# Kernel optimization log

Hardware: AMD Instinct MI355X
Metric: run time of the kernel (lower is better)

Reference implementation:

```python
import jax, jax.numpy as jnp
import numpy as np

RESO = 192
BASIS_DIM = 8
DATA_DIM = BASIS_DIM * 3 + 4  # 28
N_PTS = 2_000_000


def setup_inputs() -> dict:
    key = jax.random.key(0)
    k1, k2 = jax.random.split(key)
    # world-space points within the grid radius [-1, 1]^3
    points = jax.random.uniform(k1, (N_PTS, 3), jnp.float32, -1.0, 1.0)
    data = jax.random.normal(k2, (RESO ** 3, DATA_DIM), jnp.float32) * 0.1
    links = jnp.arange(RESO ** 3, dtype=jnp.int32).reshape(RESO, RESO, RESO)
    # _offset = 0.5*(1 - center/radius) = 0.5 ; _scaling = 0.5/radius = 0.5
    offset = jnp.full((3,), 0.5, jnp.float32)
    scaling = jnp.full((3,), 0.5, jnp.float32)
    return {"points": points, "data": data, "links": links,
            "offset": offset, "scaling": scaling}


def _fetch(data, links, ix, iy, iz):
    # sparse indirection: link < 0 means empty voxel -> all-zero channels
    lk = links[ix, iy, iz]                       # (N,) int32
    vals = data[jnp.clip(lk, 0)]                 # (N, C)
    return jnp.where((lk >= 0)[:, None], vals, 0.0)


def reference(points, data, links, offset, scaling):
    gsz_f = jnp.asarray(links.shape, jnp.float32)   # (3,)
    gsz_i = jnp.asarray(links.shape, jnp.int32)
    # world2grid then clamp to [0, size-1] (border padding, align_corners=False)
    pts = points * (scaling * gsz_f) + (offset * gsz_f - 0.5)
    pts = jnp.clip(pts, 0.0, gsz_f - 1.0)
    l = jnp.clip(pts.astype(jnp.int32), 0, gsz_i - 2)  # lower corner, (N,3)
    wb = pts - l.astype(jnp.float32)                   # frac weights
    wa = 1.0 - wb
    lx, ly, lz = l[:, 0], l[:, 1], l[:, 2]

    c000 = _fetch(data, links, lx, ly, lz)
    c001 = _fetch(data, links, lx, ly, lz + 1)
    c010 = _fetch(data, links, lx, ly + 1, lz)
    c011 = _fetch(data, links, lx, ly + 1, lz + 1)
    c100 = _fetch(data, links, lx + 1, ly, lz)
    c101 = _fetch(data, links, lx + 1, ly, lz + 1)
    c110 = _fetch(data, links, lx + 1, ly + 1, lz)
    c111 = _fetch(data, links, lx + 1, ly + 1, lz + 1)

    wz_a, wz_b = wa[:, 2:3], wb[:, 2:3]
    c00 = c000 * wz_a + c001 * wz_b
    c01 = c010 * wz_a + c011 * wz_b
    c10 = c100 * wz_a + c101 * wz_b
    c11 = c110 * wz_a + c111 * wz_b
    c0 = c00 * wa[:, 1:2] + c01 * wb[:, 1:2]
    c1 = c10 * wa[:, 1:2] + c11 * wb[:, 1:2]
    samples = c0 * wa[:, 0:1] + c1 * wb[:, 0:1]        # (N, 28)
    return samples
```

## Files before the change

### kernel.cpp

```cpp
#include <hip/hip_runtime.h>
#include <stdint.h>

#define RESO 192
#define NVOX (RESO * RESO * RESO)
#define DATA_DIM 28
#define CHUNKS 7
#define TPA 12
#define NT 1728
#define NXCD 8
#define TPX 216
#define BLOCKS_P 256

#define AS1 __attribute__((address_space(1)))
#define AS3 __attribute__((address_space(3)))


__device__ __forceinline__ float4 f4_lerp(float4 a, float4 b, float wa, float wb) {
    float4 r;
    r.x = fmaf(a.x, wa, b.x * wb);
    r.y = fmaf(a.y, wa, b.y * wb);
    r.z = fmaf(a.z, wa, b.z * wb);
    r.w = fmaf(a.w, wa, b.w * wb);
    return r;
}

__device__ __forceinline__ int point_coords(
    const float* __restrict__ points,
    const float* __restrict__ offset,
    const float* __restrict__ scaling,
    int p, int* l, float* wb)
{
    int t = 0;
#pragma unroll
    for (int i = 0; i < 3; ++i) {
        float v = fmaf(points[(size_t)p * 3 + i], scaling[i] * (float)RESO,
                       offset[i] * (float)RESO - 0.5f);
        v = fminf(fmaxf(v, 0.0f), (float)RESO - 1.0f);
        int li = (int)v;
        if (li > RESO - 2) li = RESO - 2;
        l[i] = li;
        wb[i] = v - (float)li;
        t = t * TPA + (li >> 4);
    }
    return t;
}

__device__ __forceinline__ float4 trilerp8(const float4* cv, float4 pw) {
    const float waz = 1.0f - pw.z, wbz = pw.z;
    const float way = 1.0f - pw.y, wby = pw.y;
    const float wax = 1.0f - pw.x, wbx = pw.x;
    float4 c00 = f4_lerp(cv[0], cv[1], waz, wbz);
    float4 c01 = f4_lerp(cv[2], cv[3], waz, wbz);
    float4 c10 = f4_lerp(cv[4], cv[5], waz, wbz);
    float4 c11 = f4_lerp(cv[6], cv[7], waz, wbz);
    float4 c0 = f4_lerp(c00, c01, way, wby);
    float4 c1 = f4_lerp(c10, c11, way, wby);
    return f4_lerp(c0, c1, wax, wbx);
}


__global__ void k_init_flag(int* __restrict__ flag) {
    if (threadIdx.x == 0) flag[0] = 1;
}

__global__ __launch_bounds__(256) void k_check_links(
    const int* __restrict__ links, int* __restrict__ flag)
{
    bool ok = true;
    for (int i = blockIdx.x * 256 + threadIdx.x; i < NVOX; i += gridDim.x * 256)
        ok &= (links[i] == i);
    if (!ok) atomicAnd(flag, 0);
}


__global__ __launch_bounds__(256) void k_hist(
    const float* __restrict__ points,
    const float* __restrict__ offset,
    const float* __restrict__ scaling,
    int* __restrict__ ghist,
    int n, int ppb)
{
    __shared__ int lh[NT];
    for (int i = threadIdx.x; i < NT; i += 256) lh[i] = 0;
    __syncthreads();
    const int b = blockIdx.x;
    const int lo = b * ppb;
    const int hi = min(lo + ppb, n);
    for (int p = lo + threadIdx.x; p < hi; p += 256) {
        int l[3]; float wb[3];
        const int t = point_coords(points, offset, scaling, p, l, wb);
        atomicAdd(&lh[t], 1);
    }
    __syncthreads();
    for (int i = threadIdx.x; i < NT; i += 256)
        ghist[(size_t)i * BLOCKS_P + b] = lh[i];
}

__global__ __launch_bounds__(256) void k_rowsum(
    const int* __restrict__ ghist, int* __restrict__ binsum)
{
    const int wave = (blockIdx.x * 256 + threadIdx.x) >> 6;
    const int lane = threadIdx.x & 63;
    if (wave >= NT) return;
    const int* row = ghist + (size_t)wave * BLOCKS_P;
    int s = 0;
#pragma unroll
    for (int i = 0; i < BLOCKS_P / 64; ++i) s += row[lane + i * 64];
#pragma unroll
    for (int d = 32; d > 0; d >>= 1) s += __shfl_xor(s, d, 64);
    if (lane == 0) binsum[wave] = s;
}

__global__ __launch_bounds__(1024) void k_scan_bins(
    const int* __restrict__ binsum, int* __restrict__ csum)
{
    __shared__ int buf[2][2048];
    for (int t = threadIdx.x; t < 2048; t += 1024)
        buf[0][t] = (t < NT) ? binsum[t] : 0;
    __syncthreads();
    int src = 0;
    for (int d = 1; d < 2048; d <<= 1) {
        for (int t = threadIdx.x; t < 2048; t += 1024)
            buf[src ^ 1][t] = buf[src][t] + (t >= d ? buf[src][t - d] : 0);
        __syncthreads();
        src ^= 1;
    }
    for (int t = threadIdx.x; t < NT; t += 1024)
        csum[t] = t ? buf[src][t - 1] : 0;
    if (threadIdx.x == 0) csum[NT] = buf[src][NT - 1];
}

__global__ __launch_bounds__(256) void k_scan_blocks(
    const int* __restrict__ ghist,
    const int* __restrict__ csum,
    int* __restrict__ goff)
{
    const int wave = (blockIdx.x * 256 + threadIdx.x) >> 6;
    const int lane = threadIdx.x & 63;
    if (wave >= NT) return;
    const int* row  = ghist + (size_t)wave * BLOCKS_P;
    int*       orow = goff  + (size_t)wave * BLOCKS_P;
    const int C = BLOCKS_P / 64;
    int v[C], pre[C];
    int lsum = 0;
#pragma unroll
    for (int i = 0; i < C; ++i) {
        v[i] = row[lane * C + i];
        pre[i] = lsum;
        lsum += v[i];
    }
    int incl = lsum;
#pragma unroll
    for (int d = 1; d < 64; d <<= 1) {
        int t = __shfl_up(incl, d, 64);
        if (lane >= d) incl += t;
    }
    const int excl = incl - lsum + csum[wave];
#pragma unroll
    for (int i = 0; i < C; ++i)
        orow[lane * C + i] = excl + pre[i];
}

__global__ __launch_bounds__(256) void k_scatter(
    const float* __restrict__ points,
    const float* __restrict__ offset,
    const float* __restrict__ scaling,
    const int* __restrict__ goff,
    int* __restrict__ perm,
    float4* __restrict__ pre4,
    int n, int ppb)
{
    __shared__ int cur[NT];
    const int b = blockIdx.x;
    for (int i = threadIdx.x; i < NT; i += 256)
        cur[i] = goff[(size_t)i * BLOCKS_P + b];
    __syncthreads();
    const int lo = b * ppb;
    const int hi = min(lo + ppb, n);
    for (int p = lo + threadIdx.x; p < hi; p += 256) {
        int l[3]; float wb[3];
        const int t = point_coords(points, offset, scaling, p, l, wb);
        const int slot = atomicAdd(&cur[t], 1);
        const int gbase = (l[0] * RESO + l[1]) * RESO + l[2];
        perm[slot] = p;
        pre4[slot] = make_float4(wb[0], wb[1], wb[2], __int_as_float(gbase));
    }
}


__global__ __launch_bounds__(256) void k_sample_sorted(
    const int*    __restrict__ perm,
    const float4* __restrict__ pre4,
    const int*    __restrict__ csum,
    const float*  __restrict__ data,
    const int*    __restrict__ links,
    const int*    __restrict__ flag,
    float*        __restrict__ out,
    int bpx)
{
    __shared__ __align__(16) char stage[4 * 8 * 64 * 16];
    char* wbase = stage + (threadIdx.x >> 6) * 8192;
    const int lane = threadIdx.x & 63;

    const int k = blockIdx.x & (NXCD - 1);
    const int j = blockIdx.x >> 3;
    const int lo = csum[k * TPX];
    const int hi = csum[(k + 1) * TPX];
    const int nwork = (hi - lo) * CHUNKS;
    const int stride = bpx * 256;
    const bool fast = (flag[0] != 0);
    const int dz = 1, dy = RESO, dx = RESO * RESO;
    const int offs[8] = {0, dz, dy, dy + dz, dx, dx + dz, dx + dy, dx + dy + dz};

    for (int item = j * 256 + (int)threadIdx.x; item < nwork; item += stride) {
        const int slot = lo + item / CHUNKS;
        const int c    = item % CHUNKS;
        const int p    = perm[slot];
        const float4 pw = pre4[slot];
        const int gbase = __float_as_int(pw.w);

        float4 cv[8];

        if (fast) {
            const float* bA = data + (size_t)c * 4;
#pragma unroll
            for (int q = 0; q < 8; ++q) {
                const float* g = bA + (size_t)(gbase + offs[q]) * DATA_DIM;
                __builtin_amdgcn_global_load_lds(
                    (const AS1 void*)g, (AS3 void*)(wbase + q * 1024), 16, 0, 0);
            }
            asm volatile("s_waitcnt vmcnt(0)" ::: "memory");
#pragma unroll
            for (int q = 0; q < 8; ++q)
                cv[q] = *reinterpret_cast<const float4*>(wbase + q * 1024 + lane * 16);
        } else {
            int lk[8];
#pragma unroll
            for (int q = 0; q < 8; ++q) lk[q] = links[gbase + offs[q]];
#pragma unroll
            for (int q = 0; q < 8; ++q)
                cv[q] = *reinterpret_cast<const float4*>(
                    data + (size_t)(lk[q] < 0 ? 0 : lk[q]) * DATA_DIM + (size_t)c * 4);
#pragma unroll
            for (int q = 0; q < 8; ++q)
                if (lk[q] < 0) cv[q] = make_float4(0.f, 0.f, 0.f, 0.f);
        }

        const float4 s = trilerp8(cv, pw);
        *reinterpret_cast<float4*>(out + (size_t)p * DATA_DIM + (size_t)c * 4) = s;
    }
}


__global__ __launch_bounds__(256) void k_sample_direct(
    const float* __restrict__ points,
    const float* __restrict__ data,
    const int*   __restrict__ links,
    const float* __restrict__ offset,
    const float* __restrict__ scaling,
    float*       __restrict__ out,
    int n_pts)
{
    const int tid = blockIdx.x * blockDim.x + threadIdx.x;
    const int total = n_pts * CHUNKS;
    if (tid >= total) return;
    const int p = tid / CHUNKS;
    const int c = tid - p * CHUNKS;

    int l[3]; float wb[3];
    (void)point_coords(points, offset, scaling, p, l, wb);
    const int gbase = (l[0] * RESO + l[1]) * RESO + l[2];

    const int dz = 1, dy = RESO, dx = RESO * RESO;
    int lk[8];
    lk[0] = links[gbase];
    lk[1] = links[gbase + dz];
    lk[2] = links[gbase + dy];
    lk[3] = links[gbase + dy + dz];
    lk[4] = links[gbase + dx];
    lk[5] = links[gbase + dx + dz];
    lk[6] = links[gbase + dx + dy];
    lk[7] = links[gbase + dx + dy + dz];

    float4 cv[8];
#pragma unroll
    for (int q = 0; q < 8; ++q) {
        const int idx = lk[q] < 0 ? 0 : lk[q];
        cv[q] = *reinterpret_cast<const float4*>(
            data + (size_t)idx * DATA_DIM + (size_t)c * 4);
    }
#pragma unroll
    for (int q = 0; q < 8; ++q)
        if (lk[q] < 0) cv[q] = make_float4(0.f, 0.f, 0.f, 0.f);

    float4 pw = make_float4(wb[0], wb[1], wb[2], 0.f);
    const float4 s = trilerp8(cv, pw);
    *reinterpret_cast<float4*>(out + (size_t)tid * 4) = s;
}


extern "C" void kernel_launch(void* const* d_in, const int* in_sizes, int n_in,
                              void* d_out, int out_size, void* d_ws, size_t ws_size,
                              hipStream_t stream)
{
    const float* points  = (const float*)d_in[0];
    const float* data    = (const float*)d_in[1];
    const int*   links   = (const int*)d_in[2];
    const float* offset  = (const float*)d_in[3];
    const float* scaling = (const float*)d_in[4];
    float*       out     = (float*)d_out;

    const int n_pts = in_sizes[0] / 3;

    size_t off = 0;
    auto alloc = [&](size_t bytes) {
        size_t a = off;
        off = (off + bytes + 255) & ~(size_t)255;
        return a;
    };
    const size_t o_flag   = alloc(4);
    const size_t o_ghist  = alloc((size_t)NT * BLOCKS_P * 4);
    const size_t o_goff   = alloc((size_t)NT * BLOCKS_P * 4);
    const size_t o_binsum = alloc((size_t)NT * 4);
    const size_t o_csum   = alloc((size_t)(NT + 1) * 4);
    const size_t o_perm   = alloc((size_t)n_pts * 4);
    const size_t o_pre4   = alloc((size_t)n_pts * 16);
    const size_t need = off;

    if (ws_size >= need) {
        int*    flag   = (int*)((char*)d_ws + o_flag);
        int*    ghist  = (int*)((char*)d_ws + o_ghist);
        int*    goff   = (int*)((char*)d_ws + o_goff);
        int*    binsum = (int*)((char*)d_ws + o_binsum);
        int*    csum   = (int*)((char*)d_ws + o_csum);
        int*    perm   = (int*)((char*)d_ws + o_perm);
        float4* pre4   = (float4*)((char*)d_ws + o_pre4);

        const int ppb = (n_pts + BLOCKS_P - 1) / BLOCKS_P;

        k_init_flag<<<1, 64, 0, stream>>>(flag);
        k_check_links<<<2048, 256, 0, stream>>>(links, flag);
        k_hist<<<BLOCKS_P, 256, 0, stream>>>(points, offset, scaling, ghist, n_pts, ppb);
        k_rowsum<<<(NT * 64 + 255) / 256, 256, 0, stream>>>(ghist, binsum);
        k_scan_bins<<<1, 1024, 0, stream>>>(binsum, csum);
        k_scan_blocks<<<(NT * 64 + 255) / 256, 256, 0, stream>>>(ghist, csum, goff);
        k_scatter<<<BLOCKS_P, 256, 0, stream>>>(points, offset, scaling, goff,
                                                perm, pre4, n_pts, ppb);

        const long long items_per_xcd =
            ((long long)n_pts * CHUNKS + NXCD - 1) / NXCD;
        const int bpx = (int)((items_per_xcd + 255) / 256);
        k_sample_sorted<<<bpx * NXCD, 256, 0, stream>>>(
            perm, pre4, csum, data, links, flag, out, bpx);
    } else {
        const int total = n_pts * CHUNKS;
        k_sample_direct<<<(total + 255) / 256, 256, 0, stream>>>(
            points, data, links, offset, scaling, out, n_pts);
    }
}
```

Before: 453.6 us.

## Stage 9x9x9 voxel tiles in LDS per fine bin for trilinear sampling

Points are binned into finer 8^3-voxel tiles (13824 bins), and the histogram and offset tables are transposed to a block-major layout. The per-bin scans become one thread per bin. The sampling kernel now runs one block per tile. It loads the tile's 9x9x9 voxel neighbourhood of data into LDS with coalesced float4 loads, then serves all eight corner reads from LDS instead of doing per-point global gathers. The cost is about 81KB of dynamic LDS per block, which limits occupancy, plus redundant halo loads, and the staging is not overlapped with compute.

```diff
diff --git a/kernel.cpp b/kernel.cpp
--- a/kernel.cpp
+++ b/kernel.cpp
@@ -5,14 +5,14 @@
 #define NVOX (RESO * RESO * RESO)
 #define DATA_DIM 28
 #define CHUNKS 7
-#define TPA 12
-#define NT 1728
+#define TPA 24
+#define NBIN 13824
 #define NXCD 8
-#define TPX 216
+#define BPX 1728
 #define BLOCKS_P 256
-
-#define AS1 __attribute__((address_space(1)))
-#define AS3 __attribute__((address_space(3)))
+#define ROWF 252
+#define STAGE_F (81 * ROWF)
+#define STAGE_LD (81 * (ROWF / 4))
 
 
 __device__ __forceinline__ float4 f4_lerp(float4 a, float4 b, float wa, float wb) {
@@ -40,7 +40,7 @@
         if (li > RESO - 2) li = RESO - 2;
         l[i] = li;
         wb[i] = v - (float)li;
-        t = t * TPA + (li >> 4);
+        t = t * TPA + (li >> 3);
     }
     return t;
 }
@@ -80,8 +80,8 @@
     int* __restrict__ ghist,
     int n, int ppb)
 {
-    __shared__ int lh[NT];
-    for (int i = threadIdx.x; i < NT; i += 256) lh[i] = 0;
+    __shared__ int lh[NBIN];
+    for (int i = threadIdx.x; i < NBIN; i += 256) lh[i] = 0;
     __syncthreads();
     const int b = blockIdx.x;
     const int lo = b * ppb;
@@ -92,42 +92,41 @@
         atomicAdd(&lh[t], 1);
     }
     __syncthreads();
-    for (int i = threadIdx.x; i < NT; i += 256)
-        ghist[(size_t)i * BLOCKS_P + b] = lh[i];
+    int* orow = ghist + (size_t)b * NBIN;
+    for (int i = threadIdx.x; i < NBIN; i += 256) orow[i] = lh[i];
 }
 
 __global__ __launch_bounds__(256) void k_rowsum(
     const int* __restrict__ ghist, int* __restrict__ binsum)
 {
-    const int wave = (blockIdx.x * 256 + threadIdx.x) >> 6;
-    const int lane = threadIdx.x & 63;
-    if (wave >= NT) return;
-    const int* row = ghist + (size_t)wave * BLOCKS_P;
+    const int bin = blockIdx.x * 256 + threadIdx.x;
+    if (bin >= NBIN) return;
     int s = 0;
-#pragma unroll
-    for (int i = 0; i < BLOCKS_P / 64; ++i) s += row[lane + i * 64];
-#pragma unroll
-    for (int d = 32; d > 0; d >>= 1) s += __shfl_xor(s, d, 64);
-    if (lane == 0) binsum[wave] = s;
-}
-
-__global__ __launch_bounds__(1024) void k_scan_bins(
+    for (int b = 0; b < BLOCKS_P; ++b) s += ghist[(size_t)b * NBIN + bin];
+    binsum[bin] = s;
+}
+
+__global__ __launch_bounds__(512) void k_scan_bins(
     const int* __restrict__ binsum, int* __restrict__ csum)
 {
-    __shared__ int buf[2][2048];
-    for (int t = threadIdx.x; t < 2048; t += 1024)
-        buf[0][t] = (t < NT) ? binsum[t] : 0;
-    __syncthreads();
-    int src = 0;
-    for (int d = 1; d < 2048; d <<= 1) {
-        for (int t = threadIdx.x; t < 2048; t += 1024)
-            buf[src ^ 1][t] = buf[src][t] + (t >= d ? buf[src][t - d] : 0);
+    __shared__ int vals[NBIN];
+    __shared__ int part[512];
+    const int t = threadIdx.x;
+    const int PER = NBIN / 512;
+    int s = 0;
+    for (int i = 0; i < PER; ++i) { int v = binsum[t * PER + i]; vals[t * PER + i] = v; s += v; }
+    part[t] = s;
+    __syncthreads();
+    for (int d = 1; d < 512; d <<= 1) {
+        int v = part[t];
+        int add = (t >= d) ? part[t - d] : 0;
         __syncthreads();
-        src ^= 1;
-    }
-    for (int t = threadIdx.x; t < NT; t += 1024)
-        csum[t] = t ? buf[src][t - 1] : 0;
-    if (threadIdx.x == 0) csum[NT] = buf[src][NT - 1];
+        part[t] = v + add;
+        __syncthreads();
+    }
+    int run = (t == 0) ? 0 : part[t - 1];
+    for (int i = 0; i < PER; ++i) { int v = vals[t * PER + i]; csum[t * PER + i] = run; run += v; }
+    if (t == 511) csum[NBIN] = run;
 }
 
 __global__ __launch_bounds__(256) void k_scan_blocks(
@@ -135,30 +134,13 @@
     const int* __restrict__ csum,
     int* __restrict__ goff)
 {
-    const int wave = (blockIdx.x * 256 + threadIdx.x) >> 6;
-    const int lane = threadIdx.x & 63;
-    if (wave >= NT) return;
-    const int* row  = ghist + (size_t)wave * BLOCKS_P;
-    int*       orow = goff  + (size_t)wave * BLOCKS_P;
-    const int C = BLOCKS_P / 64;
-    int v[C], pre[C];
-    int lsum = 0;
-#pragma unroll
-    for (int i = 0; i < C; ++i) {
-        v[i] = row[lane * C + i];
-        pre[i] = lsum;
-        lsum += v[i];
-    }
-    int incl = lsum;
-#pragma unroll
-    for (int d = 1; d < 64; d <<= 1) {
-        int t = __shfl_up(incl, d, 64);
-        if (lane >= d) incl += t;
-    }
-    const int excl = incl - lsum + csum[wave];
-#pragma unroll
-    for (int i = 0; i < C; ++i)
-        orow[lane * C + i] = excl + pre[i];
+    const int bin = blockIdx.x * 256 + threadIdx.x;
+    if (bin >= NBIN) return;
+    int run = csum[bin];
+    for (int b = 0; b < BLOCKS_P; ++b) {
+        goff[(size_t)b * NBIN + bin] = run;
+        run += ghist[(size_t)b * NBIN + bin];
+    }
 }
 
 __global__ __launch_bounds__(256) void k_scatter(
@@ -170,10 +152,10 @@
     float4* __restrict__ pre4,
     int n, int ppb)
 {
-    __shared__ int cur[NT];
+    __shared__ int cur[NBIN];
     const int b = blockIdx.x;
-    for (int i = threadIdx.x; i < NT; i += 256)
-        cur[i] = goff[(size_t)i * BLOCKS_P + b];
+    const int* grow = goff + (size_t)b * NBIN;
+    for (int i = threadIdx.x; i < NBIN; i += 256) cur[i] = grow[i];
     __syncthreads();
     const int lo = b * ppb;
     const int hi = min(lo + ppb, n);
@@ -181,59 +163,78 @@
         int l[3]; float wb[3];
         const int t = point_coords(points, offset, scaling, p, l, wb);
         const int slot = atomicAdd(&cur[t], 1);
-        const int gbase = (l[0] * RESO + l[1]) * RESO + l[2];
+        const unsigned lpack = ((unsigned)l[0] << 16) | ((unsigned)l[1] << 8) | (unsigned)l[2];
         perm[slot] = p;
-        pre4[slot] = make_float4(wb[0], wb[1], wb[2], __int_as_float(gbase));
-    }
-}
-
-
-__global__ __launch_bounds__(256) void k_sample_sorted(
+        pre4[slot] = make_float4(wb[0], wb[1], wb[2], __uint_as_float(lpack));
+    }
+}
+
+
+__global__ __launch_bounds__(256) void k_sample_tiled(
     const int*    __restrict__ perm,
     const float4* __restrict__ pre4,
     const int*    __restrict__ csum,
     const float*  __restrict__ data,
     const int*    __restrict__ links,
     const int*    __restrict__ flag,
-    float*        __restrict__ out,
-    int bpx)
-{
-    __shared__ __align__(16) char stage[4 * 8 * 64 * 16];
-    char* wbase = stage + (threadIdx.x >> 6) * 8192;
-    const int lane = threadIdx.x & 63;
-
-    const int k = blockIdx.x & (NXCD - 1);
-    const int j = blockIdx.x >> 3;
-    const int lo = csum[k * TPX];
-    const int hi = csum[(k + 1) * TPX];
-    const int nwork = (hi - lo) * CHUNKS;
-    const int stride = bpx * 256;
+    float*        __restrict__ out)
+{
+    extern __shared__ float lds[];
+
+    const int k   = blockIdx.x & (NXCD - 1);
+    const int j   = blockIdx.x >> 3;
+    const int bin = k * BPX + j;
+    const int bx = bin / (TPA * TPA);
+    const int by = (bin / TPA) % TPA;
+    const int bz = bin % TPA;
+    const int b0x = min(bx * 8, RESO - 9);
+    const int b0y = min(by * 8, RESO - 9);
+    const int b0z = min(bz * 8, RESO - 9);
+
     const bool fast = (flag[0] != 0);
+    const int lo = csum[bin], hi = csum[bin + 1];
+    const int items = (hi - lo) * CHUNKS;
+
+    if (fast) {
+        for (int i = threadIdx.x; i < STAGE_LD; i += 256) {
+            const int pair = i / 63;
+            const int f4   = i - pair * 63;
+            const int gx = b0x + pair / 9;
+            const int gy = b0y + (pair - (pair / 9) * 9);
+            const float* src = data + ((size_t)(gx * RESO + gy) * RESO + b0z) * DATA_DIM
+                             + (size_t)f4 * 4;
+            *reinterpret_cast<float4*>(lds + pair * ROWF + f4 * 4) =
+                *reinterpret_cast<const float4*>(src);
+        }
+    }
+    __syncthreads();
+
+    const int dzf = 28, dyf = ROWF, dxf = 9 * ROWF;
     const int dz = 1, dy = RESO, dx = RESO * RESO;
-    const int offs[8] = {0, dz, dy, dy + dz, dx, dx + dz, dx + dy, dx + dy + dz};
-
-    for (int item = j * 256 + (int)threadIdx.x; item < nwork; item += stride) {
-        const int slot = lo + item / CHUNKS;
-        const int c    = item % CHUNKS;
+
+    for (int i = threadIdx.x; i < items; i += 256) {
+        const int slot = lo + i / CHUNKS;
+        const int c    = i - (i / CHUNKS) * CHUNKS;
         const int p    = perm[slot];
         const float4 pw = pre4[slot];
-        const int gbase = __float_as_int(pw.w);
+        const unsigned lp = __float_as_uint(pw.w);
+        const int lx = lp >> 16, ly = (lp >> 8) & 255, lz = lp & 255;
 
         float4 cv[8];
-
         if (fast) {
-            const float* bA = data + (size_t)c * 4;
-#pragma unroll
-            for (int q = 0; q < 8; ++q) {
-                const float* g = bA + (size_t)(gbase + offs[q]) * DATA_DIM;
-                __builtin_amdgcn_global_load_lds(
-                    (const AS1 void*)g, (AS3 void*)(wbase + q * 1024), 16, 0, 0);
-            }
-            asm volatile("s_waitcnt vmcnt(0)" ::: "memory");
-#pragma unroll
-            for (int q = 0; q < 8; ++q)
-                cv[q] = *reinterpret_cast<const float4*>(wbase + q * 1024 + lane * 16);
+            const float* fb = lds + ((lx - b0x) * 9 + (ly - b0y)) * ROWF
+                            + (lz - b0z) * 28 + c * 4;
+            cv[0] = *reinterpret_cast<const float4*>(fb);
+            cv[1] = *reinterpret_cast<const float4*>(fb + dzf);
+            cv[2] = *reinterpret_cast<const float4*>(fb + dyf);
+            cv[3] = *reinterpret_cast<const float4*>(fb + dyf + dzf);
+            cv[4] = *reinterpret_cast<const float4*>(fb + dxf);
+            cv[5] = *reinterpret_cast<const float4*>(fb + dxf + dzf);
+            cv[6] = *reinterpret_cast<const float4*>(fb + dxf + dyf);
+            cv[7] = *reinterpret_cast<const float4*>(fb + dxf + dyf + dzf);
         } else {
+            const int gbase = (lx * RESO + ly) * RESO + lz;
+            const int offs[8] = {0, dz, dy, dy + dz, dx, dx + dz, dx + dy, dx + dy + dz};
             int lk[8];
 #pragma unroll
             for (int q = 0; q < 8; ++q) lk[q] = links[gbase + offs[q]];
@@ -319,10 +320,10 @@
         return a;
     };
     const size_t o_flag   = alloc(4);
-    const size_t o_ghist  = alloc((size_t)NT * BLOCKS_P * 4);
-    const size_t o_goff   = alloc((size_t)NT * BLOCKS_P * 4);
-    const size_t o_binsum = alloc((size_t)NT * 4);
-    const size_t o_csum   = alloc((size_t)(NT + 1) * 4);
+    const size_t o_ghist  = alloc((size_t)NBIN * BLOCKS_P * 4);
+    const size_t o_goff   = alloc((size_t)NBIN * BLOCKS_P * 4);
+    const size_t o_binsum = alloc((size_t)NBIN * 4);
+    const size_t o_csum   = alloc((size_t)(NBIN + 1) * 4);
     const size_t o_perm   = alloc((size_t)n_pts * 4);
     const size_t o_pre4   = alloc((size_t)n_pts * 16);
     const size_t need = off;
@@ -341,17 +342,14 @@
         k_init_flag<<<1, 64, 0, stream>>>(flag);
         k_check_links<<<2048, 256, 0, stream>>>(links, flag);
         k_hist<<<BLOCKS_P, 256, 0, stream>>>(points, offset, scaling, ghist, n_pts, ppb);
-        k_rowsum<<<(NT * 64 + 255) / 256, 256, 0, stream>>>(ghist, binsum);
-        k_scan_bins<<<1, 1024, 0, stream>>>(binsum, csum);
-        k_scan_blocks<<<(NT * 64 + 255) / 256, 256, 0, stream>>>(ghist, csum, goff);
+        k_rowsum<<<(NBIN + 255) / 256, 256, 0, stream>>>(ghist, binsum);
+        k_scan_bins<<<1, 512, 0, stream>>>(binsum, csum);
+        k_scan_blocks<<<(NBIN + 255) / 256, 256, 0, stream>>>(ghist, csum, goff);
         k_scatter<<<BLOCKS_P, 256, 0, stream>>>(points, offset, scaling, goff,
                                                 perm, pre4, n_pts, ppb);
 
-        const long long items_per_xcd =
-            ((long long)n_pts * CHUNKS + NXCD - 1) / NXCD;
-        const int bpx = (int)((items_per_xcd + 255) / 256);
-        k_sample_sorted<<<bpx * NXCD, 256, 0, stream>>>(
-            perm, pre4, csum, data, links, flag, out, bpx);
+        k_sample_tiled<<<NBIN, 256, STAGE_F * 4, stream>>>(
+            perm, pre4, csum, data, links, flag, out);
     } else {
         const int total = n_pts * CHUNKS;
         k_sample_direct<<<(total + 255) / 256, 256, 0, stream>>>(
```

After: 626.8 us. 1.38x slower.
